# Performance work log

Measured on AMD Instinct MI355X. Metric: run time of the kernel, lower is better.

## Reference

```python
import jax, jax.numpy as jnp
import numpy as np

D, H, E, K, N, PROJ = 512, 1024, 8, 2, 65536, 256
C = N * K // E  # expert capacity (capacity_factor=1.0 over the full token count)
LOG100 = float(np.log(100.0))


def _l2norm(v, axis=-1):
    return v / (jnp.linalg.norm(v, axis=axis, keepdims=True) + 1e-12)


def _moe(x, mask, Wp, bp, sim, temp, W1, b1, W2, b2):
    # tutel 'cosine_top' gate: cosine sim between projected tokens and expert embeddings,
    # scaled by clamped learned temperature.
    logits = _l2norm(x @ Wp + bp) @ _l2norm(sim, axis=0)
    logits = logits * jnp.exp(jnp.minimum(temp, LOG100))
    gates_all = jax.nn.softmax(logits, axis=-1)
    g, idx = jax.lax.top_k(gates_all, K)                      # [N,K]
    g = g / (jnp.sum(g, axis=-1, keepdims=True) + 1e-9)       # normalize top-k gates
    g = g * mask[:, None]                                     # zero out tokens not in this domain
    e = idx.reshape(-1)                                       # [N*K] expert id per slot
    gflat = g.reshape(-1)
    valid = jnp.repeat(mask, K)                               # [N*K]
    oh = jax.nn.one_hot(e, E, dtype=jnp.float32) * valid[:, None]
    pos = (jnp.cumsum(oh, axis=0) * oh).sum(-1).astype(jnp.int32) - 1  # slot within expert
    keep = ((pos >= 0) & (pos < C)).astype(x.dtype)           # drop overflow / masked tokens
    posc = jnp.clip(pos, 0, C - 1)
    tok = jnp.arange(N * K, dtype=jnp.int32) // K
    # dispatch -> [E,C,D]
    xd = jnp.zeros((E, C, D), x.dtype).at[e, posc].add(x[tok] * keep[:, None])
    # grouped expert FFN
    h = jax.nn.relu(jnp.einsum('ecd,edh->ech', xd, W1) + b1[:, None, :])
    y = jnp.einsum('ech,ehd->ecd', h, W2) + b2[:, None, :]
    # combine back to tokens
    out = jnp.zeros((N, D), x.dtype).at[tok].add(y[e, posc] * (gflat * keep)[:, None])
    return out


def _make_params(key):
    ks = jax.random.split(key, 4)
    Wp = jax.random.normal(ks[0], (D, PROJ), jnp.float32) * 0.02
    bp = jnp.zeros((PROJ,), jnp.float32)
    sim = jax.random.normal(ks[1], (PROJ, E), jnp.float32) * 0.02
    temp = jnp.asarray(np.log(10.0), jnp.float32)
    W1 = jax.random.normal(ks[2], (E, D, H), jnp.float32) * (1.0 / np.sqrt(D))
    b1 = jnp.zeros((E, H), jnp.float32)
    W2 = jax.random.normal(ks[3], (E, H, D), jnp.float32) * (1.0 / np.sqrt(H))
    b2 = jnp.zeros((E, D), jnp.float32)
    return Wp, bp, sim, temp, W1, b1, W2, b2


def setup_inputs():
    key = jax.random.key(0)
    kx, kl, k1, k2, k3, ksc = jax.random.split(key, 6)
    inp = {
        'x': jax.random.normal(kx, (N, D), jnp.float32),
        'domain_label': jax.random.randint(kl, (N,), 0, 2),
        'domain_scale': jax.random.normal(ksc, (1,), jnp.float32) * 0.1,
    }
    for name, k in (('sh', k1), ('day', k2), ('nt', k3)):
        Wp, bp, sim, temp, W1, b1, W2, b2 = _make_params(k)
        inp.update({name + '_Wp': Wp, name + '_bp': bp, name + '_sim': sim, name + '_temp': temp,
                    name + '_W1': W1, name + '_b1': b1, name + '_W2': W2, name + '_b2': b2})
    return inp


def reference(x, domain_label, domain_scale,
              sh_Wp, sh_bp, sh_sim, sh_temp, sh_W1, sh_b1, sh_W2, sh_b2,
              day_Wp, day_bp, day_sim, day_temp, day_W1, day_b1, day_W2, day_b2,
              nt_Wp, nt_bp, nt_sim, nt_temp, nt_W1, nt_b1, nt_W2, nt_b2):
    ones = jnp.ones((N,), jnp.float32)
    day = (domain_label == 0).astype(jnp.float32)
    night = (domain_label == 1).astype(jnp.float32)
    f_shared = _moe(x, ones, sh_Wp, sh_bp, sh_sim, sh_temp, sh_W1, sh_b1, sh_W2, sh_b2)
    f_domain = (_moe(x, day, day_Wp, day_bp, day_sim, day_temp, day_W1, day_b1, day_W2, day_b2)
                + _moe(x, night, nt_Wp, nt_bp, nt_sim, nt_temp, nt_W1, nt_b1, nt_W2, nt_b2))
    return f_shared + domain_scale * f_domain
```

## Files before the change

### kernel.cpp

```cpp
#include <hip/hip_runtime.h>

#define NTOK 65536
#define DDIM 512
#define HDIM 1024
#define NEXP 8
#define PROJ 256
#define CAP  16384
#define NSLOT (2*NTOK)
#define LOG100 4.605170185988091f

typedef __attribute__((ext_vector_type(8))) short bf16x8;
typedef __attribute__((ext_vector_type(4))) short short4v;
typedef __attribute__((ext_vector_type(4))) float f32x4;

__device__ inline float bf2f(unsigned short u){
    union { float f; unsigned int i; } c; c.i = ((unsigned int)u) << 16; return c.f;
}
__device__ inline unsigned short f2bf(float f){
    union { float f; unsigned int i; } c; c.f = f;
    unsigned int x = c.i;
    return (unsigned short)((x + 0x7fffu + ((x >> 16) & 1u)) >> 16);
}
__device__ inline void gload16(const void* g, void* lds){
    __builtin_amdgcn_global_load_lds(
        (const __attribute__((address_space(1))) unsigned int*)g,
        (__attribute__((address_space(3))) unsigned int*)lds, 16, 0, 0);
}

__global__ void init_k(const float4* __restrict__ x, ushort4* __restrict__ xb,
                       float4* __restrict__ out){
    long i = (long)blockIdx.x * 256 + threadIdx.x;
    float4 f = x[i];
    ushort4 u; u.x = f2bf(f.x); u.y = f2bf(f.y); u.z = f2bf(f.z); u.w = f2bf(f.w);
    xb[i] = u;
    out[i] = float4{0.f, 0.f, 0.f, 0.f};
}

__device__ inline void trans_body(const float* in, unsigned short* out, int R, int C){
    int rbase = blockIdx.y * 32, cbase = blockIdx.x * 32;
    if (rbase >= R || cbase >= C) return;
    __shared__ float tile[32][33];
    int tx = threadIdx.x, ty = threadIdx.y;
    #pragma unroll
    for (int i = 0; i < 4; i++)
        tile[ty + i*8][tx] = in[(long)(rbase + ty + i*8) * C + cbase + tx];
    __syncthreads();
    #pragma unroll
    for (int i = 0; i < 4; i++)
        out[(long)(cbase + ty + i*8) * R + rbase + tx] = f2bf(tile[tx][ty + i*8]);
}

__global__ __launch_bounds__(256)
void trans2_k(const float* __restrict__ W1, const float* __restrict__ W2,
              unsigned short* __restrict__ W1T, unsigned short* __restrict__ W2T)
{
    int z = blockIdx.z;
    if (z < 8) trans_body(W1 + (size_t)z*DDIM*HDIM, W1T + (size_t)z*DDIM*HDIM, DDIM, HDIM);
    else       trans_body(W2 + (size_t)(z-8)*DDIM*HDIM, W2T + (size_t)(z-8)*DDIM*HDIM, HDIM, DDIM);
}

struct W12P { const float* W1[3]; const float* W2[3]; };
__global__ __launch_bounds__(256)
void transW12all_k(W12P wp, unsigned short* __restrict__ W1T3, unsigned short* __restrict__ W2T3)
{
    int z = blockIdx.z, m = z >> 4, piece = z & 15;
    if (piece < 8)
        trans_body(wp.W1[m] + (size_t)piece*DDIM*HDIM,
                   W1T3 + ((size_t)m*8 + piece)*DDIM*HDIM, DDIM, HDIM);
    else
        trans_body(wp.W2[m] + (size_t)(piece-8)*DDIM*HDIM,
                   W2T3 + ((size_t)m*8 + piece-8)*DDIM*HDIM, HDIM, DDIM);
}

struct TpArgs { const float* Wp[3]; };
__global__ __launch_bounds__(256)
void transWp_k(TpArgs ta, unsigned short* __restrict__ WpT3)
{
    int m = blockIdx.z;
    trans_body(ta.Wp[m], WpT3 + (size_t)m*PROJ*DDIM, DDIM, PROJ);
}

struct SimArgs { const float* sim[3]; };
__global__ void simn3_k(SimArgs sa, float* __restrict__ simn3){
    __shared__ float red[256];
    const float* sim = sa.sim[blockIdx.x];
    float* simn = simn3 + (size_t)blockIdx.x * PROJ * NEXP;
    int j = threadIdx.x;
    for (int e = 0; e < NEXP; e++){
        float v = sim[j*NEXP + e];
        red[j] = v*v;
        __syncthreads();
        for (int s = 128; s > 0; s >>= 1){
            if (j < s) red[j] += red[j + s];
            __syncthreads();
        }
        float nrm = sqrtf(red[0]) + 1e-12f;
        __syncthreads();
        simn[j*NEXP + e] = v / nrm;
    }
}

struct WprodArgs { const float* Wp[3]; const float* bp[3]; };
__global__ __launch_bounds__(256)
void wprod_k(WprodArgs wa, const float* __restrict__ simn3,
             float* __restrict__ Wn3, float* __restrict__ bd3)
{
    int m = blockIdx.x;
    __shared__ float Sn[PROJ*NEXP];
    const float* Wp = wa.Wp[m];
    int t = threadIdx.x;
    for (int i = t; i < PROJ*NEXP; i += 256) Sn[i] = simn3[(size_t)m*PROJ*NEXP + i];
    __syncthreads();
    for (int r = t; r < DDIM; r += 256){
        float d[8];
        #pragma unroll
        for (int e = 0; e < 8; e++) d[e] = 0.f;
        for (int p = 0; p < PROJ; p++){
            float w = Wp[(size_t)r*PROJ + p];
            #pragma unroll
            for (int e = 0; e < 8; e++) d[e] = fmaf(w, Sn[p*8+e], d[e]);
        }
        #pragma unroll
        for (int e = 0; e < 8; e++) Wn3[((size_t)m*DDIM + r)*8 + e] = d[e];
    }
    if (t < 8){
        float s = 0.f;
        for (int p = 0; p < PROJ; p++) s = fmaf(wa.bp[m][p], Sn[p*8+t], s);
        bd3[m*8 + t] = s;
    }
}

struct PssArgs { const float* bp[3]; };
__global__ __launch_bounds__(256)
void pss_k(const unsigned short* __restrict__ WpT3, const unsigned short* __restrict__ xb,
           PssArgs pa, float* __restrict__ ssbuf)
{
    __shared__ __align__(16) short As[128*32];
    __shared__ __align__(16) short Bs[128*32];
    __shared__ float ssl[2][128];
    const int m = blockIdx.z;
    const int row0 = blockIdx.x * 128;
    const int n0 = blockIdx.y * 128;
    const unsigned short* AT = WpT3 + (size_t)m * PROJ * DDIM;
    const float* bp = pa.bp[m];

    const int t = threadIdx.x, w = t >> 6, l = t & 63;
    const int qrow = l >> 2, kc = (l & 3) * 8;
    long arowg[2], browg[2];
    #pragma unroll
    for (int q = 0; q < 2; q++){
        arowg[q] = (long)(row0 + w*32 + q*16 + qrow) * DDIM;
        browg[q] = (long)(n0   + w*32 + q*16 + qrow) * DDIM;
    }
    const int wm = (w >> 1) * 64, wn = (w & 1) * 64;
    const int fr = l & 15, fk = l >> 4;
    const int koff = fk * 8, fk4 = fk * 4;

    f32x4 acc[4][4];
    #pragma unroll
    for (int i = 0; i < 4; i++)
        #pragma unroll
        for (int j = 0; j < 4; j++) acc[i][j] = (f32x4){0.f, 0.f, 0.f, 0.f};

    for (int k0 = 0; k0 < DDIM; k0 += 32){
        __syncthreads();
        #pragma unroll
        for (int q = 0; q < 2; q++) gload16(AT + arowg[q] + k0 + kc, As + w*1024 + q*512);
        #pragma unroll
        for (int q = 0; q < 2; q++) gload16(xb + browg[q] + k0 + kc, Bs + w*1024 + q*512);
        __syncthreads();
        bf16x8 af[4], bfv[4];
        #pragma unroll
        for (int i = 0; i < 4; i++) af[i]  = *(const bf16x8*)&As[(wm + i*16 + fr)*32 + koff];
        #pragma unroll
        for (int j = 0; j < 4; j++) bfv[j] = *(const bf16x8*)&Bs[(wn + j*16 + fr)*32 + koff];
        #pragma unroll
        for (int i = 0; i < 4; i++)
            #pragma unroll
            for (int j = 0; j < 4; j++)
                acc[i][j] = __builtin_amdgcn_mfma_f32_16x16x32_bf16(af[i], bfv[j], acc[i][j], 0, 0, 0);
    }

    float part[4];
    #pragma unroll
    for (int j = 0; j < 4; j++){
        float s = 0.f;
        #pragma unroll
        for (int i = 0; i < 4; i++){
            int mc = row0 + wm + i*16 + fk4;
            float4 bb = *(const float4*)(bp + mc);
            float v0 = acc[i][j][0] + bb.x;
            float v1 = acc[i][j][1] + bb.y;
            float v2 = acc[i][j][2] + bb.z;
            float v3 = acc[i][j][3] + bb.w;
            s += v0*v0 + v1*v1 + v2*v2 + v3*v3;
        }
        s += __shfl_xor(s, 16, 64);
        s += __shfl_xor(s, 32, 64);
        part[j] = s;
    }
    if (fk == 0){
        #pragma unroll
        for (int j = 0; j < 4; j++) ssl[w >> 1][wn + j*16 + fr] = part[j];
    }
    __syncthreads();
    if (t < 128)
        ssbuf[((size_t)blockIdx.x*3 + m)*NTOK + n0 + t] = ssl[0][t] + ssl[1][t];
}

struct GfArgs { const float* tp[3]; };
__global__ __launch_bounds__(256)
void gatefin3_k(const float* __restrict__ x, const int* __restrict__ label,
                const float* __restrict__ Wn3, const float* __restrict__ bd3,
                const float* __restrict__ ssbuf, GfArgs gf,
                int* __restrict__ idx3, float* __restrict__ gw3)
{
    __shared__ float pd[3][64][26];
    const int t = threadIdx.x;
    const int tok = t & 63;
    const int qu = __builtin_amdgcn_readfirstlane(t >> 6);
    const int n = blockIdx.x * 64 + tok;

    float dots[3][8];
    #pragma unroll
    for (int m = 0; m < 3; m++)
        #pragma unroll
        for (int e = 0; e < 8; e++) dots[m][e] = 0.f;

    const float4* xp = (const float4*)(x + (size_t)n * DDIM + qu * 128);
    for (int c = 0; c < 8; c++){
        float4 xv[4];
        #pragma unroll
        for (int u = 0; u < 4; u++) xv[u] = xp[c*4 + u];
        #pragma unroll
        for (int kk = 0; kk < 16; kk++){
            float a = (kk & 2) ? ((kk & 1) ? xv[kk>>2].w : xv[kk>>2].z)
                               : ((kk & 1) ? xv[kk>>2].y : xv[kk>>2].x);
            int k = qu*128 + c*16 + kk;
            #pragma unroll
            for (int m = 0; m < 3; m++){
                const float* wr = Wn3 + ((size_t)m*DDIM + k)*8;
                float4 w0 = *(const float4*)wr;
                float4 w1 = *(const float4*)(wr + 4);
                dots[m][0] = fmaf(a, w0.x, dots[m][0]);
                dots[m][1] = fmaf(a, w0.y, dots[m][1]);
                dots[m][2] = fmaf(a, w0.z, dots[m][2]);
                dots[m][3] = fmaf(a, w0.w, dots[m][3]);
                dots[m][4] = fmaf(a, w1.x, dots[m][4]);
                dots[m][5] = fmaf(a, w1.y, dots[m][5]);
                dots[m][6] = fmaf(a, w1.z, dots[m][6]);
                dots[m][7] = fmaf(a, w1.w, dots[m][7]);
            }
        }
    }
    if (qu != 0){
        #pragma unroll
        for (int m = 0; m < 3; m++)
            #pragma unroll
            for (int e = 0; e < 8; e++) pd[qu-1][tok][m*8+e] = dots[m][e];
    }
    __syncthreads();
    if (qu == 0){
        #pragma unroll
        for (int qq = 0; qq < 3; qq++)
            #pragma unroll
            for (int m = 0; m < 3; m++)
                #pragma unroll
                for (int e = 0; e < 8; e++) dots[m][e] += pd[qq][tok][m*8+e];

        int lab = label[n];
        #pragma unroll
        for (int m = 0; m < 3; m++){
            float ss = ssbuf[(0*3+m)*(size_t)NTOK + n] + ssbuf[(1*3+m)*(size_t)NTOK + n];
            float scale = expf(fminf(gf.tp[m][0], LOG100));
            float inv = scale / (sqrtf(ss) + 1e-12f);
            float l8[8], mx = -1e30f;
            #pragma unroll
            for (int e = 0; e < 8; e++){
                l8[e] = (dots[m][e] + bd3[m*8+e]) * inv;
                mx = fmaxf(mx, l8[e]);
            }
            float g[8], s = 0.f;
            #pragma unroll
            for (int e = 0; e < 8; e++){ g[e] = expf(l8[e] - mx); s += g[e]; }
            #pragma unroll
            for (int e = 0; e < 8; e++) g[e] /= s;
            int e0 = 0; float b0 = g[0];
            #pragma unroll
            for (int e = 1; e < 8; e++) if (g[e] > b0){ b0 = g[e]; e0 = e; }
            int e1 = (e0 == 0) ? 1 : 0; float b1v = g[e1];
            #pragma unroll
            for (int e = 0; e < 8; e++) if (e != e0 && g[e] > b1v){ b1v = g[e]; e1 = e; }
            float maskv = (m == 0) ? 1.f : ((lab == m - 1) ? 1.f : 0.f);
            float s2 = b0 + b1v + 1e-9f;
            size_t base = (size_t)m * NSLOT + 2*(size_t)n;
            gw3[base]   = b0 / s2 * maskv;
            gw3[base+1] = b1v / s2 * maskv;
            idx3[base]   = e0;
            idx3[base+1] = e1;
        }
    }
}

template<int BGATHER, int OMODE>
__device__ __forceinline__
void gemm_core_t(short* As, short* Bs,
                 const unsigned short* __restrict__ AT, const unsigned short* __restrict__ Bv,
                 const float* __restrict__ bias, void* __restrict__ Cout,
                 int Kd, int Mld, int row0, int col0, int limitN,
                 const int* __restrict__ rowidx, const int* __restrict__ otok,
                 const float* __restrict__ gs)
{
    const int t = threadIdx.x;
    const int w = t >> 6, l = t & 63;
    const int qrow = l >> 2;
    const int kc = (l & 3) * 8;

    long arowg[2], browg[2];
    #pragma unroll
    for (int q = 0; q < 2; q++){
        arowg[q] = (long)(row0 + w*32 + q*16 + qrow) * Kd;
        int s = col0 + w*32 + q*16 + qrow;
        int gi = s;
        if (BGATHER) gi = (s < limitN) ? rowidx[s] : 0;
        browg[q] = (long)gi * Kd;
    }

    const int wm = (w >> 1) * 64, wn = (w & 1) * 64;
    const int fr = l & 15, fk = l >> 4;
    const int koff = fk * 8, fk4 = fk * 4;

    f32x4 acc[4][4];
    #pragma unroll
    for (int i = 0; i < 4; i++)
        #pragma unroll
        for (int j = 0; j < 4; j++) acc[i][j] = (f32x4){0.f, 0.f, 0.f, 0.f};

    for (int k0 = 0; k0 < Kd; k0 += 32){
        __syncthreads();
        #pragma unroll
        for (int q = 0; q < 2; q++) gload16(AT + arowg[q] + k0 + kc, As + w*1024 + q*512);
        #pragma unroll
        for (int q = 0; q < 2; q++) gload16(Bv + browg[q] + k0 + kc, Bs + w*1024 + q*512);
        __syncthreads();
        bf16x8 af[4], bfv[4];
        #pragma unroll
        for (int i = 0; i < 4; i++) af[i]  = *(const bf16x8*)&As[(wm + i*16 + fr)*32 + koff];
        #pragma unroll
        for (int j = 0; j < 4; j++) bfv[j] = *(const bf16x8*)&Bs[(wn + j*16 + fr)*32 + koff];
        __builtin_amdgcn_s_setprio(1);
        #pragma unroll
        for (int i = 0; i < 4; i++)
            #pragma unroll
            for (int j = 0; j < 4; j++)
                acc[i][j] = __builtin_amdgcn_mfma_f32_16x16x32_bf16(af[i], bfv[j], acc[i][j], 0, 0, 0);
        __builtin_amdgcn_s_setprio(0);
    }

    #pragma unroll
    for (int i = 0; i < 4; i++){
        const int mc = row0 + wm + i*16 + fk4;
        float4 bb = *(const float4*)(bias + mc);
        #pragma unroll
        for (int j = 0; j < 4; j++){
            int s = col0 + wn + j*16 + fr;
            if (s < limitN){
                if (OMODE == 1){
                    ushort4 u;
                    u.x = f2bf(fmaxf(acc[i][j][0] + bb.x, 0.f));
                    u.y = f2bf(fmaxf(acc[i][j][1] + bb.y, 0.f));
                    u.z = f2bf(fmaxf(acc[i][j][2] + bb.z, 0.f));
                    u.w = f2bf(fmaxf(acc[i][j][3] + bb.w, 0.f));
                    *(ushort4*)((unsigned short*)Cout + (long)s * Mld + mc) = u;
                } else {
                    int tk = otok[s];
                    float g = gs[s];
                    float* op = (float*)Cout + (long)tk * Mld + mc;
                    float4 c = *(const float4*)op;
                    c.x += g * (acc[i][j][0] + bb.x);
                    c.y += g * (acc[i][j][1] + bb.y);
                    c.z += g * (acc[i][j][2] + bb.z);
                    c.w += g * (acc[i][j][3] + bb.w);
                    *(float4*)op = c;
                }
            }
        }
    }
}

template<int BGATHER, int OMODE>
__device__ __forceinline__
void gemm_core_t64(short* As, short* Bs,
                   const unsigned short* __restrict__ AT, const unsigned short* __restrict__ Bv,
                   const float* __restrict__ bias, void* __restrict__ Cout,
                   int Kd, int Mld, int row0, int col0, int limitN,
                   const int* __restrict__ rowidx, const int* __restrict__ otok,
                   const float* __restrict__ gs)
{
    const int t = threadIdx.x;
    const int w = t >> 6, l = t & 63;
    const int qrow = l >> 2;
    const int seg = (l & 3) * 8;

    long arowg[2], browg[2];
    #pragma unroll
    for (int q = 0; q < 2; q++){
        arowg[q] = (long)(row0 + w*32 + q*16 + qrow) * Kd;
        int s = col0 + w*32 + q*16 + qrow;
        int gi = s;
        if (BGATHER) gi = (s < limitN) ? rowidx[s] : 0;
        browg[q] = (long)gi * Kd;
    }

    const int wm = (w >> 1) * 64, wn = (w & 1) * 64;
    const int fr = l & 15, fk = l >> 4;
    const int koff = fk * 8, fk4 = fk * 4;

    f32x4 acc[4][4];
    #pragma unroll
    for (int i = 0; i < 4; i++)
        #pragma unroll
        for (int j = 0; j < 4; j++) acc[i][j] = (f32x4){0.f, 0.f, 0.f, 0.f};

    for (int k0 = 0; k0 < Kd; k0 += 64){
        __syncthreads();
        #pragma unroll
        for (int ks = 0; ks < 2; ks++)
            #pragma unroll
            for (int q = 0; q < 2; q++)
                gload16(AT + arowg[q] + k0 + ks*32 + seg, As + ks*4096 + w*1024 + q*512);
        #pragma unroll
        for (int ks = 0; ks < 2; ks++)
            #pragma unroll
            for (int q = 0; q < 2; q++)
                gload16(Bv + browg[q] + k0 + ks*32 + seg, Bs + ks*4096 + w*1024 + q*512);
        __syncthreads();
        #pragma unroll
        for (int ks = 0; ks < 2; ks++){
            bf16x8 af[4], bfv[4];
            #pragma unroll
            for (int i = 0; i < 4; i++) af[i]  = *(const bf16x8*)&As[ks*4096 + (wm + i*16 + fr)*32 + koff];
            #pragma unroll
            for (int j = 0; j < 4; j++) bfv[j] = *(const bf16x8*)&Bs[ks*4096 + (wn + j*16 + fr)*32 + koff];
            __builtin_amdgcn_s_setprio(1);
            #pragma unroll
            for (int i = 0; i < 4; i++)
                #pragma unroll
                for (int j = 0; j < 4; j++)
                    acc[i][j] = __builtin_amdgcn_mfma_f32_16x16x32_bf16(af[i], bfv[j], acc[i][j], 0, 0, 0);
            __builtin_amdgcn_s_setprio(0);
        }
    }

    #pragma unroll
    for (int i = 0; i < 4; i++){
        const int mc = row0 + wm + i*16 + fk4;
        float4 bb = *(const float4*)(bias + mc);
        #pragma unroll
        for (int j = 0; j < 4; j++){
            int s = col0 + wn + j*16 + fr;
            if (s < limitN){
                if (OMODE == 1){
                    ushort4 u;
                    u.x = f2bf(fmaxf(acc[i][j][0] + bb.x, 0.f));
                    u.y = f2bf(fmaxf(acc[i][j][1] + bb.y, 0.f));
                    u.z = f2bf(fmaxf(acc[i][j][2] + bb.z, 0.f));
                    u.w = f2bf(fmaxf(acc[i][j][3] + bb.w, 0.f));
                    *(ushort4*)((unsigned short*)Cout + (long)s * Mld + mc) = u;
                } else {
                    int tk = otok[s];
                    float g = gs[s];
                    float* op = (float*)Cout + (long)tk * Mld + mc;
                    float4 c = *(const float4*)op;
                    c.x += g * (acc[i][j][0] + bb.x);
                    c.y += g * (acc[i][j][1] + bb.y);
                    c.z += g * (acc[i][j][2] + bb.z);
                    c.w += g * (acc[i][j][3] + bb.w);
                    *(float4*)op = c;
                }
            }
        }
    }
}

__device__ __forceinline__
void gemm_core_y64(short* lds,
                   const unsigned short* __restrict__ AT, const unsigned short* __restrict__ Bv,
                   const float* __restrict__ bias, float* __restrict__ out,
                   int row0, int col0, int limitN,
                   const int* __restrict__ otok, const float* __restrict__ gs)
{
    short* As = lds;
    short* Bs = lds + 4096;
    const int t = threadIdx.x, w = t >> 6, l = t & 63;
    const int seg = (l & 3) * 8;

    const long arow = (long)(row0 + w*16 + (l >> 2)) * HDIM;
    long brow[2];
    #pragma unroll
    for (int hh = 0; hh < 2; hh++)
        brow[hh] = (long)(col0 + w*32 + hh*16 + (l >> 2)) * HDIM;

    const int wm = (w >> 1) * 32, wn = (w & 1) * 64;
    const int fr = l & 15, fk = l >> 4;
    const int koff = fk * 8, fk4 = fk * 4;

    f32x4 acc[2][4];
    #pragma unroll
    for (int i = 0; i < 2; i++)
        #pragma unroll
        for (int j = 0; j < 4; j++) acc[i][j] = (f32x4){0.f, 0.f, 0.f, 0.f};

    for (int k0 = 0; k0 < HDIM; k0 += 64){
        __syncthreads();
        #pragma unroll
        for (int ks = 0; ks < 2; ks++)
            gload16(AT + arow + k0 + ks*32 + seg, As + ks*2048 + w*512);
        #pragma unroll
        for (int ks = 0; ks < 2; ks++)
            #pragma unroll
            for (int hh = 0; hh < 2; hh++)
                gload16(Bv + brow[hh] + k0 + ks*32 + seg, Bs + ks*4096 + w*1024 + hh*512);
        __syncthreads();
        #pragma unroll
        for (int ks = 0; ks < 2; ks++){
            bf16x8 af[2], bfv[4];
            #pragma unroll
            for (int i = 0; i < 2; i++)
                af[i] = *(const bf16x8*)&As[ks*2048 + (wm + i*16 + fr)*32 + koff];
            #pragma unroll
            for (int j = 0; j < 4; j++)
                bfv[j] = *(const bf16x8*)&Bs[ks*4096 + (wn + j*16 + fr)*32 + koff];
            __builtin_amdgcn_s_setprio(1);
            #pragma unroll
            for (int i = 0; i < 2; i++)
                #pragma unroll
                for (int j = 0; j < 4; j++)
                    acc[i][j] = __builtin_amdgcn_mfma_f32_16x16x32_bf16(af[i], bfv[j], acc[i][j], 0, 0, 0);
            __builtin_amdgcn_s_setprio(0);
        }
    }

    #pragma unroll
    for (int i = 0; i < 2; i++){
        const int mc = row0 + wm + i*16 + fk4;
        float4 bb = *(const float4*)(bias + mc);
        #pragma unroll
        for (int j = 0; j < 4; j++){
            int s = col0 + wn + j*16 + fr;
            if (s < limitN){
                int tk = otok[s];
                float g = gs[s];
                float* op = out + (long)tk * DDIM + mc;
                float4 c = *(const float4*)op;
                c.x += g * (acc[i][j][0] + bb.x);
                c.y += g * (acc[i][j][1] + bb.y);
                c.z += g * (acc[i][j][2] + bb.z);
                c.w += g * (acc[i][j][3] + bb.w);
                *(float4*)op = c;
            }
        }
    }
}

template<int BGATHER, int OMODE>
__global__ __launch_bounds__(256)
void mgemm3_k(const unsigned short* __restrict__ AT, const unsigned short* __restrict__ Bv,
              const float* __restrict__ bias, void* __restrict__ Cout,
              int Kd, int Mld,
              const int* __restrict__ rowidx, const int* __restrict__ otok,
              const float* __restrict__ gs, const int* __restrict__ cntp, int cnti)
{
    __shared__ __align__(16) short As[128*32];
    __shared__ __align__(16) short Bs[128*32];
    int limit = cntp[cnti]; if (limit > CAP) limit = CAP;
    int row0 = blockIdx.x * 128, col0 = blockIdx.y * 128;
    if (col0 >= limit) return;
    gemm_core_t<BGATHER, OMODE>(As, Bs, AT, Bv, bias, Cout, Kd, Mld,
                                row0, col0, limit, rowidx, otok, gs);
}

struct FfnP { const float* b1[3]; const float* b2[3]; };
__global__ __launch_bounds__(256)
void ffnA_k(const unsigned short* __restrict__ xb,
            const unsigned short* __restrict__ W1T3, const unsigned short* __restrict__ W2T3,
            FfnP fp, unsigned short* __restrict__ h0, unsigned short* __restrict__ h1,
            float* __restrict__ out,
            const int* __restrict__ tok3, const float* __restrict__ gslot3,
            const int* __restrict__ cntk3, int ge)
{
    __shared__ __align__(16) short lds[16384];
    const int bx = blockIdx.x, by = blockIdx.y;
    const int col0 = bx * 128;
    if (by < 8){
        if (ge >= 24) return;
        int m = ge >> 3, e = ge & 7;
        int limit = cntk3[m*16 + e]; if (limit > CAP) limit = CAP;
        if (col0 >= limit) return;
        unsigned short* hd = (ge & 1) ? h1 : h0;
        gemm_core_t64<1, 1>(lds, lds + 8192,
                            W1T3 + ((size_t)(m*8+e))*HDIM*DDIM, xb, fp.b1[m] + (size_t)e*HDIM,
                            hd, DDIM, HDIM, by*128, col0, limit,
                            tok3 + ((size_t)m*NEXP + e)*CAP, nullptr, nullptr);
    } else {
        int gy = ge - 1; if (gy < 0) return;
        int m = gy >> 3, e = gy & 7;
        int limit = cntk3[m*16 + e]; if (limit > CAP) limit = CAP;
        if (col0 >= limit) return;
        const unsigned short* hs = (gy & 1) ? h1 : h0;
        gemm_core_y64(lds, W2T3 + ((size_t)(m*8+e))*DDIM*HDIM, hs, fp.b2[m] + (size_t)e*DDIM,
                      out, (by-8)*64, col0, limit,
                      tok3 + ((size_t)m*NEXP + e)*CAP, gslot3 + ((size_t)m*NEXP + e)*CAP);
    }
}

__global__ __launch_bounds__(256)
void ffnD_k(const unsigned short* __restrict__ xb,
            const unsigned short* __restrict__ W1T3, const unsigned short* __restrict__ W2T3,
            FfnP fp, unsigned short* __restrict__ h0, unsigned short* __restrict__ h1,
            unsigned short* __restrict__ h2, unsigned short* __restrict__ h3,
            float* __restrict__ out,
            const int* __restrict__ tok3, const float* __restrict__ gslot3,
            const int* __restrict__ cntk3, int s)
{
    __shared__ __align__(16) short lds[16384];
    const int bx = blockIdx.x, by = blockIdx.y;
    const int col0 = bx * 128;
    if (by < 16){
        if (s >= 8) return;
        int m = (by < 8) ? 1 : 2;
        int g = m*NEXP + s;
        int limit = cntk3[m*16 + s]; if (limit > CAP) limit = CAP;
        if (col0 >= limit) return;
        unsigned short* hd = (m == 1) ? ((s & 1) ? h1 : h0) : ((s & 1) ? h3 : h2);
        gemm_core_t64<1, 1>(lds, lds + 8192,
                            W1T3 + (size_t)g*HDIM*DDIM, xb, fp.b1[m] + (size_t)s*HDIM,
                            hd, DDIM, HDIM, (by & 7)*128, col0, limit,
                            tok3 + (size_t)g*CAP, nullptr, nullptr);
    } else {
        int m, e; const unsigned short* hs_;
        if (s == 0){
            if (by >= 24) return;
            m = 0; e = 7; hs_ = h1;
        } else {
            m = (by < 24) ? 1 : 2;
            e = s - 1;
            hs_ = (m == 1) ? ((e & 1) ? h1 : h0) : ((e & 1) ? h3 : h2);
        }
        int g = m*NEXP + e;
        int limit = cntk3[m*16 + e]; if (limit > CAP) limit = CAP;
        if (col0 >= limit) return;
        gemm_core_y64(lds, W2T3 + (size_t)g*DDIM*HDIM, hs_, fp.b2[m] + (size_t)e*DDIM,
                      out, ((by - 16) & 7)*64, col0, limit,
                      tok3 + (size_t)g*CAP, gslot3 + (size_t)g*CAP);
    }
}

__global__ __launch_bounds__(256)
void ffnB_k(const unsigned short* __restrict__ xb,
            const unsigned short* __restrict__ W1T, const float* __restrict__ b1,
            const unsigned short* __restrict__ W2T, const float* __restrict__ b2,
            unsigned short* __restrict__ h0, unsigned short* __restrict__ h1,
            float* __restrict__ out,
            const int* __restrict__ tok, const float* __restrict__ gslot,
            const int* __restrict__ cntk, int eh)
{
    __shared__ __align__(16) short lds[16384];
    const int bx = blockIdx.x, by = blockIdx.y;
    const int col0 = bx * 128;
    if (by < 8){
        if (eh > 7) return;
        int limit = cntk[eh]; if (limit > CAP) limit = CAP;
        if (col0 >= limit) return;
        unsigned short* hd = (eh & 1) ? h1 : h0;
        gemm_core_t64<1, 1>(lds, lds + 8192,
                            W1T + (size_t)eh*HDIM*DDIM, xb, b1 + (size_t)eh*HDIM,
                            hd, DDIM, HDIM, by*128, col0, limit,
                            tok + (size_t)eh*CAP, nullptr, nullptr);
    } else {
        int ey = eh - 1; if (ey < 0) return;
        int limit = cntk[ey]; if (limit > CAP) limit = CAP;
        if (col0 >= limit) return;
        const unsigned short* hs = (ey & 1) ? h1 : h0;
        gemm_core_y64(lds, W2T + (size_t)ey*DDIM*HDIM, hs, b2 + (size_t)ey*DDIM,
                      out, (by-8)*64, col0, limit,
                      tok + (size_t)ey*CAP, gslot + (size_t)ey*CAP);
    }
}

__global__ __launch_bounds__(1024)
void rank_count3_k(const int* __restrict__ idx3, const int* __restrict__ label,
                   int* __restrict__ bcnt3)
{
    __shared__ int c[NEXP];
    const int m = blockIdx.y;
    const int* idx = idx3 + (size_t)m * NSLOT;
    int t = threadIdx.x;
    if (t < NEXP) c[t] = 0;
    __syncthreads();
    int s = blockIdx.x * 1024 + t;
    int n = s >> 1;
    int e = idx[s];
    bool valid = (m == 0) || (label[n] == m - 1);
    if (valid) atomicAdd(&c[e], 1);
    __syncthreads();
    if (t < NEXP) bcnt3[((size_t)m*128 + blockIdx.x)*NEXP + t] = c[t];
}

__global__ void rank_scan3_k(const int* __restrict__ bcnt3, int* __restrict__ boff3,
                             int* __restrict__ cntk3)
{
    int m = blockIdx.x, e = threadIdx.x;
    if (e < NEXP){
        int run = 0;
        for (int b = 0; b < NSLOT/1024; b++){
            boff3[((size_t)m*128 + b)*NEXP + e] = run;
            run += bcnt3[((size_t)m*128 + b)*NEXP + e];
        }
        cntk3[m*16 + e] = run < CAP ? run : CAP;
    }
}

__global__ __launch_bounds__(1024)
void rank_assign3_k(const int* __restrict__ idx3, const int* __restrict__ label,
                    const int* __restrict__ boff3, const float* __restrict__ gw3,
                    const float* __restrict__ dscale,
                    int* __restrict__ tok3, float* __restrict__ gs3)
{
    __shared__ int wcnt[16][NEXP];
    __shared__ int woff[16][NEXP];
    const int m = blockIdx.y;
    const int* idx = idx3 + (size_t)m * NSLOT;
    const float* gw = gw3 + (size_t)m * NSLOT;
    int t = threadIdx.x;
    int s = blockIdx.x * 1024 + t;
    int n = s >> 1;
    int e = idx[s];
    bool valid = (m == 0) || (label[n] == m - 1);
    int w = t >> 6, lane = t & 63;
    unsigned long long lt = (lane == 0) ? 0ull : ((1ull << lane) - 1ull);
    int myrank = 0;
    #pragma unroll
    for (int ei = 0; ei < NEXP; ei++){
        unsigned long long bal = __ballot(valid && (e == ei));
        if (ei == e) myrank = __popcll(bal & lt);
        if (lane == 0) wcnt[w][ei] = __popcll(bal);
    }
    __syncthreads();
    if (t < NEXP){
        int run = boff3[((size_t)m*128 + blockIdx.x)*NEXP + t];
        for (int w2 = 0; w2 < 16; w2++){
            woff[w2][t] = run;
            run += wcnt[w2][t];
        }
    }
    __syncthreads();
    int pos = woff[w][e] + myrank;
    bool keep = valid && (pos < CAP);
    if (keep){
        float scale = (m > 0) ? dscale[0] : 1.f;
        tok3[((size_t)m*NEXP + e)*CAP + pos] = n;
        gs3[((size_t)m*NEXP + e)*CAP + pos] = gw[s] * scale;
    }
}

extern "C" void kernel_launch(void* const* d_in, const int* in_sizes, int n_in,
                              void* d_out, int out_size, void* d_ws, size_t ws_size,
                              hipStream_t stream)
{
    (void)in_sizes; (void)n_in; (void)out_size;
    const float* x      = (const float*)d_in[0];
    const int*   label  = (const int*)  d_in[1];
    const float* dscale = (const float*)d_in[2];
    float* out = (float*)d_out;

    const size_t XB  = (size_t)NTOK * DDIM * 2;
    const size_t HS  = (size_t)CAP * HDIM * 2;
    const size_t WPT = (size_t)3 * PROJ * DDIM * 2;
    const size_t SS  = (size_t)2 * 3 * NTOK * 4;
    const size_t WN  = (size_t)3 * DDIM * 8 * 4;
    const size_t SMALL = WPT + SS + WN + 256 +
                         (size_t)3*PROJ*NEXP*4 +
                         (size_t)3*NSLOT*4*2 +
                         (size_t)3*NEXP*CAP*4*2 +
                         (size_t)3*128*NEXP*4*2 + 256;
    const size_t W12A = (size_t)2 * 3 * NEXP * DDIM * HDIM * 2;
    const size_t W12B = (size_t)2 * NEXP * DDIM * HDIM * 2;
    const size_t common = XB + HS + SMALL;

    int tier;
    if      (ws_size >= common + 3*HS + W12A) tier = 0;
    else if (ws_size >= common + HS + W12A)   tier = 1;
    else if (ws_size >= common + HS + W12B)   tier = 2;
    else if (ws_size >= common + W12B)        tier = 3;
    else return;

    char* p = (char*)d_ws;
    unsigned short* xb   = (unsigned short*)p; p += XB;
    unsigned short* h0   = (unsigned short*)p; p += HS;
    unsigned short* WpT3 = (unsigned short*)p; p += WPT;
    float* ssbuf = (float*)p;  p += SS;
    float* Wn3   = (float*)p;  p += WN;
    float* bd3   = (float*)p;  p += 256;
    float* simn3 = (float*)p;  p += (size_t)3*PROJ*NEXP*4;
    int*   idx3  = (int*)p;    p += (size_t)3*NSLOT*4;
    float* gw3   = (float*)p;  p += (size_t)3*NSLOT*4;
    int*   tok3  = (int*)p;    p += (size_t)3*NEXP*CAP*4;
    float* gslot3= (float*)p;  p += (size_t)3*NEXP*CAP*4;
    int*   bcnt3 = (int*)p;    p += (size_t)3*128*NEXP*4;
    int*   boff3 = (int*)p;    p += (size_t)3*128*NEXP*4;
    int*   cntk3 = (int*)p;    p += 256;
    unsigned short* h1 = nullptr;
    unsigned short* h2 = nullptr;
    unsigned short* h3 = nullptr;
    if (tier <= 2){ h1 = (unsigned short*)p; p += HS; }
    if (tier == 0){ h2 = (unsigned short*)p; p += HS; h3 = (unsigned short*)p; p += HS; }
    unsigned short* Wbuf = (unsigned short*)p;

    SimArgs sa; TpArgs ta; WprodArgs wa; PssArgs pa; GfArgs gf; W12P wp; FfnP fp;
    for (int m = 0; m < 3; m++){
        ta.Wp[m] = (const float*)d_in[3 + 8*m + 0];
        wa.Wp[m] = ta.Wp[m];
        wa.bp[m] = (const float*)d_in[3 + 8*m + 1];
        pa.bp[m] = wa.bp[m];
        sa.sim[m] = (const float*)d_in[3 + 8*m + 2];
        gf.tp[m] = (const float*)d_in[3 + 8*m + 3];
        wp.W1[m] = (const float*)d_in[3 + 8*m + 4];
        fp.b1[m] = (const float*)d_in[3 + 8*m + 5];
        wp.W2[m] = (const float*)d_in[3 + 8*m + 6];
        fp.b2[m] = (const float*)d_in[3 + 8*m + 7];
    }

    init_k<<<dim3(NTOK*DDIM/4/256), dim3(256), 0, stream>>>(
        (const float4*)x, (ushort4*)xb, (float4*)out);
    simn3_k<<<dim3(3), dim3(256), 0, stream>>>(sa, simn3);
    transWp_k<<<dim3(PROJ/32, DDIM/32, 3), dim3(32,8), 0, stream>>>(ta, WpT3);
    wprod_k<<<dim3(3), dim3(256), 0, stream>>>(wa, simn3, Wn3, bd3);
    pss_k<<<dim3(2, NTOK/128, 3), dim3(256), 0, stream>>>(WpT3, xb, pa, ssbuf);
    gatefin3_k<<<dim3(NTOK/64), dim3(256), 0, stream>>>(
        x, label, Wn3, bd3, ssbuf, gf, idx3, gw3);

    rank_count3_k<<<dim3(NSLOT/1024, 3), dim3(1024), 0, stream>>>(idx3, label, bcnt3);
    rank_scan3_k<<<dim3(3), dim3(64), 0, stream>>>(bcnt3, boff3, cntk3);
    rank_assign3_k<<<dim3(NSLOT/1024, 3), dim3(1024), 0, stream>>>(
        idx3, label, boff3, gw3, dscale, tok3, gslot3);

    if (tier <= 1){
        unsigned short* W1T3 = Wbuf;
        unsigned short* W2T3 = Wbuf + (size_t)3*NEXP*DDIM*HDIM;
        transW12all_k<<<dim3(32, 32, 48), dim3(32,8), 0, stream>>>(wp, W1T3, W2T3);
        if (tier == 0){
            for (int ge = 0; ge < 8; ge++)
                ffnA_k<<<dim3(128, 16), 256, 0, stream>>>(
                    xb, W1T3, W2T3, fp, h0, h1, out, tok3, gslot3, cntk3, ge);
            for (int s = 0; s <= 8; s++)
                ffnD_k<<<dim3(128, 32), 256, 0, stream>>>(
                    xb, W1T3, W2T3, fp, h0, h1, h2, h3, out, tok3, gslot3, cntk3, s);
        } else {
            for (int ge = 0; ge <= 24; ge++)
                ffnA_k<<<dim3(128, 16), 256, 0, stream>>>(
                    xb, W1T3, W2T3, fp, h0, h1, out, tok3, gslot3, cntk3, ge);
        }
    } else {
        unsigned short* W1T = Wbuf;
        unsigned short* W2T = Wbuf + (size_t)NEXP*DDIM*HDIM;
        for (int m = 0; m < 3; m++){
            trans2_k<<<dim3(32, 32, 16), dim3(32,8), 0, stream>>>(wp.W1[m], wp.W2[m], W1T, W2T);
            const int* tokm = tok3 + (size_t)m*NEXP*CAP;
            const float* gsm = gslot3 + (size_t)m*NEXP*CAP;
            const int* cntm = cntk3 + m*16;
            if (tier == 2){
                for (int eh = 0; eh <= 8; eh++)
                    ffnB_k<<<dim3(128, 16), 256, 0, stream>>>(
                        xb, W1T, fp.b1[m], W2T, fp.b2[m], h0, h1, out, tokm, gsm, cntm, eh);
            } else {
                for (int e = 0; e < NEXP; e++){
                    mgemm3_k<1, 1><<<dim3(HDIM/128, CAP/128), 256, 0, stream>>>(
                        W1T + (size_t)e*HDIM*DDIM, xb, fp.b1[m] + (size_t)e*HDIM, h0,
                        DDIM, HDIM, tokm + (size_t)e*CAP, nullptr, nullptr, cntm, e);
                    mgemm3_k<0, 3><<<dim3(DDIM/128, CAP/128), 256, 0, stream>>>(
                        W2T + (size_t)e*DDIM*HDIM, h0, fp.b2[m] + (size_t)e*DDIM, out,
                        HDIM, DDIM, nullptr, tokm + (size_t)e*CAP, gsm + (size_t)e*CAP, cntm, e);
                }
            }
        }
    }
}
```

Baseline: 1.694 ms.

## Replace per-expert FFN launches with a table-driven 13-step job schedule

Replaces the ffnA/ffnD launch sequences (17 launches) with a generic ffnG kernel driven by a host-side job table of 13 launches. Each launch runs up to four jobs, mixing first-layer GEMMs for upcoming experts with second-layer GEMMs for earlier ones, and rotates through four h buffers. Fewer launches, plus keeping W1 and W2 work in flight together, aim to cut launch gaps and fill the GPU better. It depends on the hand-written schedule keeping every h buffer's write ahead of its read, with no reuse hazard across launches.

Result: faster. 1.643 ms (-3.0%).

```diff
diff --git a/kernel.cpp b/kernel.cpp
--- a/kernel.cpp
+++ b/kernel.cpp
@@ -580,7 +580,41 @@
                                 row0, col0, limit, rowidx, otok, gs);
 }
 
+struct JobsArg { int4 j[4]; };
 struct FfnP { const float* b1[3]; const float* b2[3]; };
+__global__ __launch_bounds__(256)
+void ffnG_k(const unsigned short* __restrict__ xb,
+            const unsigned short* __restrict__ W1T3, const unsigned short* __restrict__ W2T3,
+            FfnP fp,
+            unsigned short* __restrict__ hb0, unsigned short* __restrict__ hb1,
+            unsigned short* __restrict__ hb2, unsigned short* __restrict__ hb3,
+            float* __restrict__ out,
+            const int* __restrict__ tok3, const float* __restrict__ gslot3,
+            const int* __restrict__ cntk3, JobsArg ja)
+{
+    __shared__ __align__(16) short lds[16384];
+    const int bx = blockIdx.x;
+    const int ji = blockIdx.y >> 3, sub = blockIdx.y & 7;
+    const int4 J = ja.j[ji];
+    if (J.x > 1) return;
+    const int m = J.y, e = J.z;
+    unsigned short* hbuf = (J.w == 0) ? hb0 : (J.w == 1) ? hb1 : (J.w == 2) ? hb2 : hb3;
+    const int g = m*NEXP + e;
+    int limit = cntk3[m*16 + e]; if (limit > CAP) limit = CAP;
+    const int col0 = bx * 128;
+    if (col0 >= limit) return;
+    if (J.x == 0){
+        gemm_core_t64<1, 1>(lds, lds + 8192,
+                            W1T3 + (size_t)g*HDIM*DDIM, xb, fp.b1[m] + (size_t)e*HDIM,
+                            hbuf, DDIM, HDIM, sub*128, col0, limit,
+                            tok3 + (size_t)g*CAP, nullptr, nullptr);
+    } else {
+        gemm_core_y64(lds, W2T3 + (size_t)g*DDIM*HDIM, hbuf, fp.b2[m] + (size_t)e*DDIM,
+                      out, sub*64, col0, limit,
+                      tok3 + (size_t)g*CAP, gslot3 + (size_t)g*CAP);
+    }
+}
+
 __global__ __launch_bounds__(256)
 void ffnA_k(const unsigned short* __restrict__ xb,
             const unsigned short* __restrict__ W1T3, const unsigned short* __restrict__ W2T3,
@@ -615,48 +649,6 @@
 }
 
 __global__ __launch_bounds__(256)
-void ffnD_k(const unsigned short* __restrict__ xb,
-            const unsigned short* __restrict__ W1T3, const unsigned short* __restrict__ W2T3,
-            FfnP fp, unsigned short* __restrict__ h0, unsigned short* __restrict__ h1,
-            unsigned short* __restrict__ h2, unsigned short* __restrict__ h3,
-            float* __restrict__ out,
-            const int* __restrict__ tok3, const float* __restrict__ gslot3,
-            const int* __restrict__ cntk3, int s)
-{
-    __shared__ __align__(16) short lds[16384];
-    const int bx = blockIdx.x, by = blockIdx.y;
-    const int col0 = bx * 128;
-    if (by < 16){
-        if (s >= 8) return;
-        int m = (by < 8) ? 1 : 2;
-        int g = m*NEXP + s;
-        int limit = cntk3[m*16 + s]; if (limit > CAP) limit = CAP;
-        if (col0 >= limit) return;
-        unsigned short* hd = (m == 1) ? ((s & 1) ? h1 : h0) : ((s & 1) ? h3 : h2);
-        gemm_core_t64<1, 1>(lds, lds + 8192,
-                            W1T3 + (size_t)g*HDIM*DDIM, xb, fp.b1[m] + (size_t)s*HDIM,
-                            hd, DDIM, HDIM, (by & 7)*128, col0, limit,
-                            tok3 + (size_t)g*CAP, nullptr, nullptr);
-    } else {
-        int m, e; const unsigned short* hs_;
-        if (s == 0){
-            if (by >= 24) return;
-            m = 0; e = 7; hs_ = h1;
-        } else {
-            m = (by < 24) ? 1 : 2;
-            e = s - 1;
-            hs_ = (m == 1) ? ((e & 1) ? h1 : h0) : ((e & 1) ? h3 : h2);
-        }
-        int g = m*NEXP + e;
-        int limit = cntk3[m*16 + e]; if (limit > CAP) limit = CAP;
-        if (col0 >= limit) return;
-        gemm_core_y64(lds, W2T3 + (size_t)g*DDIM*HDIM, hs_, fp.b2[m] + (size_t)e*DDIM,
-                      out, ((by - 16) & 7)*64, col0, limit,
-                      tok3 + (size_t)g*CAP, gslot3 + (size_t)g*CAP);
-    }
-}
-
-__global__ __launch_bounds__(256)
 void ffnB_k(const unsigned short* __restrict__ xb,
             const unsigned short* __restrict__ W1T, const float* __restrict__ b1,
             const unsigned short* __restrict__ W2T, const float* __restrict__ b2,
@@ -850,12 +842,29 @@
         unsigned short* W2T3 = Wbuf + (size_t)3*NEXP*DDIM*HDIM;
         transW12all_k<<<dim3(32, 32, 48), dim3(32,8), 0, stream>>>(wp, W1T3, W2T3);
         if (tier == 0){
-            for (int ge = 0; ge < 8; ge++)
-                ffnA_k<<<dim3(128, 16), 256, 0, stream>>>(
-                    xb, W1T3, W2T3, fp, h0, h1, out, tok3, gslot3, cntk3, ge);
-            for (int s = 0; s <= 8; s++)
-                ffnD_k<<<dim3(128, 32), 256, 0, stream>>>(
-                    xb, W1T3, W2T3, fp, h0, h1, h2, h3, out, tok3, gslot3, cntk3, s);
+            static const int S[13][4][4] = {
+                {{0,0,0,0},{0,0,1,1},{9,0,0,0},{9,0,0,0}},
+                {{0,0,2,2},{0,0,3,3},{1,0,0,0},{1,0,1,1}},
+                {{0,0,4,0},{0,0,5,1},{1,0,2,2},{1,0,3,3}},
+                {{0,0,6,2},{0,0,7,3},{1,0,4,0},{1,0,5,1}},
+                {{0,1,0,0},{0,2,0,1},{1,0,6,2},{1,0,7,3}},
+                {{0,1,1,2},{0,2,1,3},{1,1,0,0},{1,2,0,1}},
+                {{0,1,2,0},{0,2,2,1},{1,1,1,2},{1,2,1,3}},
+                {{0,1,3,2},{0,2,3,3},{1,1,2,0},{1,2,2,1}},
+                {{0,1,4,0},{0,2,4,1},{1,1,3,2},{1,2,3,3}},
+                {{0,1,5,2},{0,2,5,3},{1,1,4,0},{1,2,4,1}},
+                {{0,1,6,0},{0,2,6,1},{1,1,5,2},{1,2,5,3}},
+                {{0,1,7,2},{0,2,7,3},{1,1,6,0},{1,2,6,1}},
+                {{1,1,7,2},{1,2,7,3},{9,0,0,0},{9,0,0,0}},
+            };
+            static const int NJ[13] = {2,4,4,4,4,4,4,4,4,4,4,4,2};
+            for (int d = 0; d < 13; d++){
+                JobsArg ja;
+                for (int i = 0; i < 4; i++)
+                    ja.j[i] = make_int4(S[d][i][0], S[d][i][1], S[d][i][2], S[d][i][3]);
+                ffnG_k<<<dim3(128, 8*NJ[d]), 256, 0, stream>>>(
+                    xb, W1T3, W2T3, fp, h0, h1, h2, h3, out, tok3, gslot3, cntk3, ja);
+            }
         } else {
             for (int ge = 0; ge <= 24; ge++)
                 ffnA_k<<<dim3(128, 16), 256, 0, stream>>>(
```
